# Kernel tuning notes

Hardware: AMD Instinct MI355X
Metric: run time of the kernel (lower is better)

The kernel has to match this reference:

```python
import jax, jax.numpy as jnp
from jax import lax
import numpy as np

N_PATTS, D_PATTS, L_PATTS = 64, 16, 64
L_OUT = L_PATTS  # module sets l_out = l_patts in both branches
RHO = 0.1
W = RHO ** (1.0 / L_PATTS)  # per-step decay weight
BIG = 1e30  # stands in for +inf at DP boundaries (avoids inf*0 nans)


def _dtw_matrix(x, patts, w):
    """Weighted-DTW DP matrix.
    x: (B, d, T), patts: (P, d, L) -> D: (B, P, L, T)
    D[i,j] = dist[i,j] + w * min(D[i-1,j], D[i,j-1], D[i-1,j-1]),
    with out-of-range predecessors = +inf and D[0,0] = dist[0,0].
    dist is the euclidean distance between x[:, :, j] and patts[:, :, i].
    """
    B, d, T = x.shape
    P, _, L = patts.shape
    x2 = jnp.sum(x * x, axis=1)              # (B, T)
    p2 = jnp.sum(patts * patts, axis=1)      # (P, L)
    xp = jnp.einsum('bdt,pdl->btpl', x, patts)  # (B, T, P, L)
    sq = x2[:, :, None, None] + p2[None, None, :, :] - 2.0 * xp
    dist = jnp.sqrt(jnp.maximum(sq, 1e-12))  # (B, T, P, L)
    dist_t = jnp.transpose(dist, (1, 0, 2, 3))  # (T, B, P, L) scan over time

    def col_step(prev_col, d_col):
        # prev_col = D[:, j-1] of shape (B, P, L); d_col = dist column (B, P, L)
        shifted = jnp.concatenate(
            [jnp.full_like(prev_col[..., :1], BIG), prev_col[..., :-1]], axis=-1)
        c = jnp.minimum(prev_col, shifted)  # min(D[i,j-1], D[i-1,j-1]) per i

        def cell(d_prev, inp):
            dist_i, c_i = inp              # each (B, P)
            m = jnp.minimum(d_prev, c_i)   # min over the 3 predecessors
            val = dist_i + jnp.where(m >= BIG * 0.5, 0.0, w * m)
            return val, val

        init = jnp.full(prev_col.shape[:2], BIG, prev_col.dtype)  # D[-1, j]
        _, col = lax.scan(
            cell, init,
            (jnp.moveaxis(d_col, -1, 0), jnp.moveaxis(c, -1, 0)))  # over i
        col = jnp.moveaxis(col, 0, -1)  # (B, P, L)
        return col, col

    init_col = jnp.full((B, P, L), BIG, dist.dtype)  # D[:, -1] = inf
    _, cols = lax.scan(col_step, init_col, dist_t)   # (T, B, P, L)
    return jnp.transpose(cols, (1, 2, 3, 0))         # (B, P, L, T)


def setup_inputs() -> dict:
    key = jax.random.key(0)
    kx, kp = jax.random.split(key)
    x = jax.random.normal(kx, (16, D_PATTS, 1024), dtype=jnp.float32)
    patts = jax.random.normal(kp, (N_PATTS, D_PATTS, L_PATTS), dtype=jnp.float32)
    return {"x": x, "patts": patts}


def reference(x, patts):
    D = _dtw_matrix(x, patts, W)          # (B, P, L, T)
    return D[:, :, :, -L_OUT:]            # last l_out time steps
```

## Files before the change

### kernel.cpp

```cpp
#include <hip/hip_runtime.h>
#include <math.h>

typedef _Float16 half8 __attribute__((ext_vector_type(8)));
typedef _Float16 h2 __attribute__((ext_vector_type(2)));
typedef float    f32x4 __attribute__((ext_vector_type(4)));
typedef unsigned int u32;
typedef unsigned long long u64;
typedef unsigned short u16;

#define BIGV 1e30f

__device__ __forceinline__ u32 dpp_shr1(u32 oldv, u32 src) {
  return (u32)__builtin_amdgcn_update_dpp((int)oldv, (int)src, 0x138, 0xF, 0xF, false);
}
__device__ __forceinline__ float cvtlo(u32 v) {
  union { u16 u; _Float16 h; } c; c.u = (u16)v; return (float)c.h;
}
__device__ __forceinline__ u16 f2h(float f) {
  union { _Float16 h; u16 u; } c; c.h = (_Float16)f; return c.u;
}
__device__ __forceinline__ u32 pkrtz(float a, float b) {
  auto v = __builtin_amdgcn_cvt_pkrtz(a, b);
  union { decltype(v) h; u32 u; } c; c.h = v; return c.u;
}
__device__ __forceinline__ u32 funnel16(u32 hi, u32 lo, u32 sh) {
  return (u32)(((((u64)hi) << 32) | (u64)lo) >> sh);
}
__device__ __forceinline__ h2 as_h2(u32 u) { union { u32 u; h2 h; } x; x.u = u; return x.h; }

__global__ __launch_bounds__(512) void dtw_pc(
    const float* __restrict__ x,
    const float* __restrict__ patts,
    float* __restrict__ out,
    float w) {
  __shared__ uint4 xsq[2050];
  __shared__ uint2 ring2[4 * 2304];
  __shared__ float obuf[4 * 1024];
  __shared__ u16   x2h16[1024];

  const int tid = threadIdx.x, lane = tid & 63, wv = tid >> 6;
  const int b = blockIdx.x >> 4, pg = blockIdx.x & 15;
  const int role = wv >> 2, pr = wv & 3;
  const int p = pg * 4 + pr;
  const int le = lane & 15, kq = lane >> 4;

  {
    const float* xb = x + b * (16 * 1024);
    u16* xh = (u16*)xsq;
    for (int idx = tid; idx < 16384; idx += 512) {
      int d = idx >> 10, t = idx & 1023;
      xh[t * 16 + d] = f2h(xb[idx]);
    }
    if (tid == 0) { xsq[2048] = make_uint4(0,0,0,0); xsq[2049] = make_uint4(0,0,0,0); }
    __syncthreads();
    for (int t = tid; t < 1024; t += 512) {
      uint4 a0 = xsq[2 * t], a1 = xsq[2 * t + 1];
      float s2 = __builtin_amdgcn_fdot2(as_h2(a0.x), as_h2(a0.x), 0.f, false);
      s2 = __builtin_amdgcn_fdot2(as_h2(a0.y), as_h2(a0.y), s2, false);
      s2 = __builtin_amdgcn_fdot2(as_h2(a0.z), as_h2(a0.z), s2, false);
      s2 = __builtin_amdgcn_fdot2(as_h2(a0.w), as_h2(a0.w), s2, false);
      s2 = __builtin_amdgcn_fdot2(as_h2(a1.x), as_h2(a1.x), s2, false);
      s2 = __builtin_amdgcn_fdot2(as_h2(a1.y), as_h2(a1.y), s2, false);
      s2 = __builtin_amdgcn_fdot2(as_h2(a1.z), as_h2(a1.z), s2, false);
      s2 = __builtin_amdgcn_fdot2(as_h2(a1.w), as_h2(a1.w), s2, false);
      x2h16[t] = f2h(s2);
    }
  }
  __syncthreads();

  if (role == 0) {
    half8 bf[4];
    {
      const float* pp = patts + p * (16 * 64);
#pragma unroll
      for (int nb = 0; nb < 4; ++nb) {
        float pv[8]; float part = 0.f;
#pragma unroll
        for (int j = 0; j < 8; ++j) {
          float f = (kq < 2) ? pp[(8 * kq + j) * 64 + nb * 16 + le] : 0.f;
          pv[j] = f; part = fmaf(f, f, part);
        }
        part += __shfl_xor(part, 16, 64);
        part += __shfl_xor(part, 32, 64);
        u32 wd0 = pkrtz(-2.f * pv[0], -2.f * pv[1]);
        u32 wd1 = pkrtz(-2.f * pv[2], -2.f * pv[3]);
        u32 wd2 = pkrtz(-2.f * pv[4], -2.f * pv[5]);
        u32 wd3 = pkrtz(-2.f * pv[6], -2.f * pv[7]);
        if (kq == 2) { wd0 = 0x3C00u | ((u32)f2h(part) << 16); wd1 = 0; wd2 = 0; wd3 = 0; }
        union { uint4 q; half8 h; } bu; bu.q = make_uint4(wd0, wd1, wd2, wd3);
        bf[nb] = bu.h;
      }
    }
    int colp = 8 * kq;
    const int wpbase = pr * 2304 + 36 * le;

#define PRODUCE(T0) { \
    int aidx_ = (kq < 2) ? (2 * ((T0) + le) + kq) : 2048; \
    uint4 aq_ = xsq[aidx_]; \
    u32 x2b_ = (u32)x2h16[(T0) + le]; \
    aq_.x = (kq == 2) ? (x2b_ | 0x3C000000u) : aq_.x; \
    union { uint4 q; half8 h; } au_; au_.q = aq_; \
    int wb_ = wpbase + (colp >> 3); \
    bool mir_ = colp < 32; \
    _Pragma("unroll") \
    for (int nb_ = 0; nb_ < 4; ++nb_) { \
      f32x4 c_ = {0.f, 0.f, 0.f, 0.f}; \
      c_ = __builtin_amdgcn_mfma_f32_16x16x32_f16(au_.h, bf[nb_], c_, 0, 0, 0); \
      float d0_ = __builtin_amdgcn_sqrtf(fmaxf(c_[0], 1e-12f)); \
      float d1_ = __builtin_amdgcn_sqrtf(fmaxf(c_[1], 1e-12f)); \
      float d2_ = __builtin_amdgcn_sqrtf(fmaxf(c_[2], 1e-12f)); \
      float d3_ = __builtin_amdgcn_sqrtf(fmaxf(c_[3], 1e-12f)); \
      uint2 st_; st_.x = pkrtz(d0_, d1_); st_.y = pkrtz(d2_, d3_); \
      ring2[wb_ + 576 * nb_] = st_; \
      if (mir_) ring2[wb_ + 576 * nb_ + 32] = st_; \
    } \
    colp = (colp + 32) & 255; }

    PRODUCE(0); PRODUCE(16);
    __syncthreads();
#pragma unroll 1
    for (int k = 0; k < 31; ++k) {
      PRODUCE(32 * k + 32);
      PRODUCE(32 * k + 48);
      __syncthreads();
    }
    __syncthreads(); __syncthreads(); __syncthreads();

  } else {
    const int rcbase = pr * 2304 + 36 * lane;
    int colc = (((0 - lane) >> 2) << 3) & 255;
    const int ph = (0 - lane) & 3;
    const u32 shv = (u32)((ph & 1) * 16);
    const bool sel2 = (ph & 2) != 0;
    float prev = BIGV, shA = BIGV, shB = BIGV;
    const int bigbits = __float_as_int(BIGV);
    float* obf = obuf + pr * 1024;
    float* obw = obf + lane * 16;
    float* oprow = out + ((b * 64 + p) * 64 + lane) * 64;
    int nextq = 240;

#define LOADQ(Q0,Q1,Q2,Q3,Q4) { int ci_ = rcbase + (colc >> 3); \
    Q0 = ring2[ci_];     Q1 = ring2[ci_ + 1]; Q2 = ring2[ci_ + 2]; \
    Q3 = ring2[ci_ + 3]; Q4 = ring2[ci_ + 4]; \
    colc = (colc + 32) & 255; }

#define SHIFT(curv) { shB = shA; \
    shA = __int_as_float((int)dpp_shr1((u32)bigbits, (u32)__float_as_int(curv))); \
    prev = (curv); }

#define STEP_PRO(S, D) { float dist_ = (D); \
    float m_ = fminf(fminf(prev, shA), shB); \
    float ms_ = (m_ >= 0.5e30f) ? 0.f : m_; \
    float val_ = fmaf(w, ms_, dist_); \
    int t_ = (S) - lane; float cur_ = (t_ >= 0) ? val_ : BIGV; \
    SHIFT(cur_); }

#define STEP_MAIN(S, D) { float dist_ = (D); \
    float m_ = fminf(fminf(prev, shA), shB); \
    float cur_ = fmaf(w, m_, dist_); \
    SHIFT(cur_); }

#define STEP_EPI(S, D) { float dist_ = (D); \
    float m_ = fminf(fminf(prev, shA), shB); \
    float val_ = fmaf(w, m_, dist_); \
    int t_ = (S) - lane; float cur_ = (t_ <= 1023) ? val_ : BIGV; \
    if ((u32)(t_ - 960) < 64u) obw[t_ & 15] = val_; \
    SHIFT(cur_); }

#define FLUSHQ(SQ) { \
    if (nextq < 256 && 4 * nextq + 3 <= (SQ) - 1 - lane - 4) { \
      float4 v_ = *(const float4*)&obf[lane * 16 + ((nextq & 3) << 2)]; \
      *(float4*)(oprow + (nextq << 2) - 960) = v_; ++nextq; \
    } }

#define EXTRACT8(Q0, Q1, Q2, Q3, Q4) \
    u32 W0_ = sel2 ? Q0.y : Q0.x, W1_ = sel2 ? Q1.x : Q0.y, \
        W2_ = sel2 ? Q1.y : Q1.x, W3_ = sel2 ? Q2.x : Q1.y, \
        W4_ = sel2 ? Q2.y : Q2.x, W5_ = sel2 ? Q3.x : Q2.y, \
        W6_ = sel2 ? Q3.y : Q3.x, W7_ = sel2 ? Q4.x : Q3.y, \
        W8_ = sel2 ? Q4.y : Q4.x; \
    u32 A0 = funnel16(W1_, W0_, shv), A1 = funnel16(W2_, W1_, shv), \
        A2 = funnel16(W3_, W2_, shv), A3 = funnel16(W4_, W3_, shv), \
        A4 = funnel16(W5_, W4_, shv), A5 = funnel16(W6_, W5_, shv), \
        A6 = funnel16(W7_, W6_, shv), A7 = funnel16(W8_, W7_, shv);

#define S16(S0, STP) \
    STP((S0)+0,  cvtlo(A0)); STP((S0)+1,  cvtlo(A0 >> 16)); \
    STP((S0)+2,  cvtlo(A1)); STP((S0)+3,  cvtlo(A1 >> 16)); \
    STP((S0)+4,  cvtlo(A2)); STP((S0)+5,  cvtlo(A2 >> 16)); \
    STP((S0)+6,  cvtlo(A3)); STP((S0)+7,  cvtlo(A3 >> 16)); \
    STP((S0)+8,  cvtlo(A4)); STP((S0)+9,  cvtlo(A4 >> 16)); \
    STP((S0)+10, cvtlo(A5)); STP((S0)+11, cvtlo(A5 >> 16)); \
    STP((S0)+12, cvtlo(A6)); STP((S0)+13, cvtlo(A6 >> 16)); \
    STP((S0)+14, cvtlo(A7)); STP((S0)+15, cvtlo(A7 >> 16));

#define SET_EPI(S0) \
    FLUSHQ((S0)+0);  STEP_EPI((S0)+0,  cvtlo(A0)); STEP_EPI((S0)+1,  cvtlo(A0 >> 16)); \
                     STEP_EPI((S0)+2,  cvtlo(A1)); STEP_EPI((S0)+3,  cvtlo(A1 >> 16)); \
    FLUSHQ((S0)+4);  STEP_EPI((S0)+4,  cvtlo(A2)); STEP_EPI((S0)+5,  cvtlo(A2 >> 16)); \
                     STEP_EPI((S0)+6,  cvtlo(A3)); STEP_EPI((S0)+7,  cvtlo(A3 >> 16)); \
    FLUSHQ((S0)+8);  STEP_EPI((S0)+8,  cvtlo(A4)); STEP_EPI((S0)+9,  cvtlo(A4 >> 16)); \
                     STEP_EPI((S0)+10, cvtlo(A5)); STEP_EPI((S0)+11, cvtlo(A5 >> 16)); \
    FLUSHQ((S0)+12); STEP_EPI((S0)+12, cvtlo(A6)); STEP_EPI((S0)+13, cvtlo(A6 >> 16)); \
                     STEP_EPI((S0)+14, cvtlo(A7)); STEP_EPI((S0)+15, cvtlo(A7 >> 16));

    __syncthreads();
#pragma unroll 1
    for (int k = 0; k < 2; ++k) {
      uint2 q0,q1,q2,q3,q4, r0,r1,r2,r3,r4;
      LOADQ(q0,q1,q2,q3,q4);
      LOADQ(r0,r1,r2,r3,r4);
      int s0 = 32 * k;
      { EXTRACT8(q0,q1,q2,q3,q4); S16(s0, STEP_PRO); }
      { EXTRACT8(r0,r1,r2,r3,r4); S16(s0 + 16, STEP_PRO); }
      __syncthreads();
    }
#pragma unroll 1
    for (int k = 2; k < 30; ++k) {
      uint2 q0,q1,q2,q3,q4, r0,r1,r2,r3,r4;
      LOADQ(q0,q1,q2,q3,q4);
      LOADQ(r0,r1,r2,r3,r4);
      int s0 = 32 * k;
      { EXTRACT8(q0,q1,q2,q3,q4); S16(s0, STEP_MAIN); }
      { EXTRACT8(r0,r1,r2,r3,r4); S16(s0 + 16, STEP_MAIN); }
      __syncthreads();
    }
#pragma unroll 1
    for (int k = 30; k < 34; ++k) {
      uint2 q0,q1,q2,q3,q4, r0,r1,r2,r3,r4;
      LOADQ(q0,q1,q2,q3,q4);
      LOADQ(r0,r1,r2,r3,r4);
      int s0 = 32 * k;
      { EXTRACT8(q0,q1,q2,q3,q4); SET_EPI(s0); }
      { EXTRACT8(r0,r1,r2,r3,r4); SET_EPI(s0 + 16); }
      __syncthreads();
    }
#pragma unroll
    for (int rr = 0; rr < 4; ++rr) {
      if (nextq < 256) {
        float4 v_ = *(const float4*)&obf[lane * 16 + ((nextq & 3) << 2)];
        *(float4*)(oprow + (nextq << 2) - 960) = v_; ++nextq;
      }
    }
  }
}

extern "C" void kernel_launch(void* const* d_in, const int* in_sizes, int n_in,
                              void* d_out, int out_size, void* d_ws, size_t ws_size,
                              hipStream_t stream) {
  const float* x     = (const float*)d_in[0];
  const float* patts = (const float*)d_in[1];
  float* out         = (float*)d_out;
  const float w = (float)exp(log(0.1) / 64.0);
  dim3 grid(256), block(512);
  hipLaunchKernelGGL(dtw_pc, grid, block, 0, stream, x, patts, out, w);
}
```

Measured before the change: 43.75 us.

## Prefetch next ring chunk in consumer and pad ring stride to avoid bank conflicts

The consumer waves now load the next 32-column chunk of the distance ring into a second register set while computing on the current one, giving software double buffering of LDS reads. The producer runs one phase further ahead to keep that lookahead valid. The ring row stride changes from 36 to 37 uint2 elements to spread LDS accesses across banks. This costs more registers in the consumer path and a deeper producer/consumer schedule that must stay correct with the ring wraparound.

```diff
diff --git a/kernel.cpp b/kernel.cpp
--- a/kernel.cpp
+++ b/kernel.cpp
@@ -9,6 +9,7 @@
 typedef unsigned short u16;
 
 #define BIGV 1e30f
+#define RSTR 37
 
 __device__ __forceinline__ u32 dpp_shr1(u32 oldv, u32 src) {
   return (u32)__builtin_amdgcn_update_dpp((int)oldv, (int)src, 0x138, 0xF, 0xF, false);
@@ -28,13 +29,13 @@
 }
 __device__ __forceinline__ h2 as_h2(u32 u) { union { u32 u; h2 h; } x; x.u = u; return x.h; }
 
-__global__ __launch_bounds__(512) void dtw_pc(
+__global__ __launch_bounds__(512) void dtw_pc2(
     const float* __restrict__ x,
     const float* __restrict__ patts,
     float* __restrict__ out,
     float w) {
   __shared__ uint4 xsq[2050];
-  __shared__ uint2 ring2[4 * 2304];
+  __shared__ uint2 ring2[4 * 64 * RSTR];
   __shared__ float obuf[4 * 1024];
   __shared__ u16   x2h16[1024];
 
@@ -92,7 +93,7 @@
       }
     }
     int colp = 8 * kq;
-    const int wpbase = pr * 2304 + 36 * le;
+    const int wpbase = pr * (64 * RSTR) + RSTR * le;
 
 #define PRODUCE(T0) { \
     int aidx_ = (kq < 2) ? (2 * ((T0) + le) + kq) : 2048; \
@@ -111,23 +112,23 @@
       float d2_ = __builtin_amdgcn_sqrtf(fmaxf(c_[2], 1e-12f)); \
       float d3_ = __builtin_amdgcn_sqrtf(fmaxf(c_[3], 1e-12f)); \
       uint2 st_; st_.x = pkrtz(d0_, d1_); st_.y = pkrtz(d2_, d3_); \
-      ring2[wb_ + 576 * nb_] = st_; \
-      if (mir_) ring2[wb_ + 576 * nb_ + 32] = st_; \
+      ring2[wb_ + (16 * RSTR) * nb_] = st_; \
+      if (mir_) ring2[wb_ + (16 * RSTR) * nb_ + 32] = st_; \
     } \
     colp = (colp + 32) & 255; }
 
-    PRODUCE(0); PRODUCE(16);
+    PRODUCE(0); PRODUCE(16); PRODUCE(32); PRODUCE(48);
     __syncthreads();
 #pragma unroll 1
-    for (int k = 0; k < 31; ++k) {
-      PRODUCE(32 * k + 32);
-      PRODUCE(32 * k + 48);
+    for (int k = 0; k < 30; ++k) {
+      PRODUCE(32 * k + 64);
+      PRODUCE(32 * k + 80);
       __syncthreads();
     }
-    __syncthreads(); __syncthreads(); __syncthreads();
+    __syncthreads(); __syncthreads(); __syncthreads(); __syncthreads();
 
   } else {
-    const int rcbase = pr * 2304 + 36 * lane;
+    const int rcbase = pr * (64 * RSTR) + RSTR * lane;
     int colc = (((0 - lane) >> 2) << 3) & 255;
     const int ph = (0 - lane) & 3;
     const u32 shv = (u32)((ph & 1) * 16);
@@ -194,6 +195,8 @@
     STP((S0)+12, cvtlo(A6)); STP((S0)+13, cvtlo(A6 >> 16)); \
     STP((S0)+14, cvtlo(A7)); STP((S0)+15, cvtlo(A7 >> 16));
 
+#define SET_PRO(S0)  S16(S0, STEP_PRO)
+#define SET_MAIN(S0) S16(S0, STEP_MAIN)
 #define SET_EPI(S0) \
     FLUSHQ((S0)+0);  STEP_EPI((S0)+0,  cvtlo(A0)); STEP_EPI((S0)+1,  cvtlo(A0 >> 16)); \
                      STEP_EPI((S0)+2,  cvtlo(A1)); STEP_EPI((S0)+3,  cvtlo(A1 >> 16)); \
@@ -204,37 +207,29 @@
     FLUSHQ((S0)+12); STEP_EPI((S0)+12, cvtlo(A6)); STEP_EPI((S0)+13, cvtlo(A6 >> 16)); \
                      STEP_EPI((S0)+14, cvtlo(A7)); STEP_EPI((S0)+15, cvtlo(A7 >> 16));
 
+#define PHASE(C0,C1,C2,C3,C4,C5,C6,C7,C8,C9, L0,L1,L2,L3,L4,L5,L6,L7,L8,L9, S0, SETM) { \
+    LOADQ(L0,L1,L2,L3,L4); LOADQ(L5,L6,L7,L8,L9); \
+    { EXTRACT8(C0,C1,C2,C3,C4); SETM(S0); } \
+    { EXTRACT8(C5,C6,C7,C8,C9); SETM((S0)+16); } \
+    __syncthreads(); }
+
     __syncthreads();
+    uint2 a0,a1,a2,a3,a4,a5,a6,a7,a8,a9;
+    uint2 b0,b1,b2,b3,b4,b5,b6,b7,b8,b9;
+    LOADQ(a0,a1,a2,a3,a4); LOADQ(a5,a6,a7,a8,a9);
+
+    PHASE(a0,a1,a2,a3,a4,a5,a6,a7,a8,a9, b0,b1,b2,b3,b4,b5,b6,b7,b8,b9, 0,  SET_PRO);
+    PHASE(b0,b1,b2,b3,b4,b5,b6,b7,b8,b9, a0,a1,a2,a3,a4,a5,a6,a7,a8,a9, 32, SET_PRO);
 #pragma unroll 1
-    for (int k = 0; k < 2; ++k) {
-      uint2 q0,q1,q2,q3,q4, r0,r1,r2,r3,r4;
-      LOADQ(q0,q1,q2,q3,q4);
-      LOADQ(r0,r1,r2,r3,r4);
-      int s0 = 32 * k;
-      { EXTRACT8(q0,q1,q2,q3,q4); S16(s0, STEP_PRO); }
-      { EXTRACT8(r0,r1,r2,r3,r4); S16(s0 + 16, STEP_PRO); }
-      __syncthreads();
-    }
-#pragma unroll 1
-    for (int k = 2; k < 30; ++k) {
-      uint2 q0,q1,q2,q3,q4, r0,r1,r2,r3,r4;
-      LOADQ(q0,q1,q2,q3,q4);
-      LOADQ(r0,r1,r2,r3,r4);
-      int s0 = 32 * k;
-      { EXTRACT8(q0,q1,q2,q3,q4); S16(s0, STEP_MAIN); }
-      { EXTRACT8(r0,r1,r2,r3,r4); S16(s0 + 16, STEP_MAIN); }
-      __syncthreads();
-    }
-#pragma unroll 1
-    for (int k = 30; k < 34; ++k) {
-      uint2 q0,q1,q2,q3,q4, r0,r1,r2,r3,r4;
-      LOADQ(q0,q1,q2,q3,q4);
-      LOADQ(r0,r1,r2,r3,r4);
-      int s0 = 32 * k;
-      { EXTRACT8(q0,q1,q2,q3,q4); SET_EPI(s0); }
-      { EXTRACT8(r0,r1,r2,r3,r4); SET_EPI(s0 + 16); }
-      __syncthreads();
-    }
+    for (int j = 1; j < 15; ++j) {
+      PHASE(a0,a1,a2,a3,a4,a5,a6,a7,a8,a9, b0,b1,b2,b3,b4,b5,b6,b7,b8,b9, 64*j,      SET_MAIN);
+      PHASE(b0,b1,b2,b3,b4,b5,b6,b7,b8,b9, a0,a1,a2,a3,a4,a5,a6,a7,a8,a9, 64*j + 32, SET_MAIN);
+    }
+    PHASE(a0,a1,a2,a3,a4,a5,a6,a7,a8,a9, b0,b1,b2,b3,b4,b5,b6,b7,b8,b9, 960,  SET_EPI);
+    PHASE(b0,b1,b2,b3,b4,b5,b6,b7,b8,b9, a0,a1,a2,a3,a4,a5,a6,a7,a8,a9, 992,  SET_EPI);
+    PHASE(a0,a1,a2,a3,a4,a5,a6,a7,a8,a9, b0,b1,b2,b3,b4,b5,b6,b7,b8,b9, 1024, SET_EPI);
+    PHASE(b0,b1,b2,b3,b4,b5,b6,b7,b8,b9, a0,a1,a2,a3,a4,a5,a6,a7,a8,a9, 1056, SET_EPI);
+
 #pragma unroll
     for (int rr = 0; rr < 4; ++rr) {
       if (nextq < 256) {
@@ -253,5 +248,5 @@
   float* out         = (float*)d_out;
   const float w = (float)exp(log(0.1) / 64.0);
   dim3 grid(256), block(512);
-  hipLaunchKernelGGL(dtw_pc, grid, block, 0, stream, x, patts, out, w);
-}
+  hipLaunchKernelGGL(dtw_pc2, grid, block, 0, stream, x, patts, out, w);
+}
```

After: 44.77 us. 2.3% more time.
